# Optimization experiments

Measured on AMD Instinct MI355X. Metric: run time of the kernel, lower is better.

## Reference

```python
import jax, jax.numpy as jnp
import numpy as np

B, S, T = 64, 128, 64
HD, VS, VT = 1024, 32000, 32000


def setup_inputs() -> dict:
    key = jax.random.key(0)
    ks = jax.random.split(key, 20)
    p = lambda k, shape: (jax.random.normal(k, shape, jnp.float32) * 0.02)
    return {
        "src_nums": jax.random.randint(ks[0], (B, S), 0, VS, dtype=jnp.int32),
        "tgt_nums": jax.random.randint(ks[1], (B, T), 0, VT, dtype=jnp.int32),
        "src_emb": p(ks[2], (VS, HD)),
        "tgt_emb": p(ks[3], (VT, HD)),
        "enc_Wx1": p(ks[4], (HD, 4 * HD)),
        "enc_Wh1": p(ks[5], (HD, 4 * HD)),
        "enc_b1": jnp.zeros((4 * HD,), jnp.float32),
        "enc_Wx2": p(ks[6], (HD, 4 * HD)),
        "enc_Wh2": p(ks[7], (HD, 4 * HD)),
        "enc_b2": jnp.zeros((4 * HD,), jnp.float32),
        "dec_Wx": p(ks[8], (HD, 4 * HD)),
        "dec_Wh": p(ks[9], (HD, 4 * HD)),
        "dec_b": jnp.zeros((4 * HD,), jnp.float32),
        "dec_h0": p(ks[10], (1, HD)),
        "dec_m0": p(ks[11], (1, HD)),
        "Wt": p(ks[12], (2 * HD, HD)),
        "bt": jnp.zeros((HD,), jnp.float32),
        "Wo": p(ks[13], (HD, VT)),
        "bo": jnp.zeros((VT,), jnp.float32),
    }


def _lstm_cell(x, h, c, Wx, Wh, b):
    g = x @ Wx + h @ Wh + b            # [B, 4H], gate order i,f,g,o
    i, f, gg, o = jnp.split(g, 4, axis=-1)
    c = jax.nn.sigmoid(f) * c + jax.nn.sigmoid(i) * jnp.tanh(gg)
    h = jax.nn.sigmoid(o) * jnp.tanh(c)
    return h, c


def reference(src_nums, tgt_nums, src_emb, tgt_emb,
              enc_Wx1, enc_Wh1, enc_b1, enc_Wx2, enc_Wh2, enc_b2,
              dec_Wx, dec_Wh, dec_b, dec_h0, dec_m0, Wt, bt, Wo, bo):
    Bb, Ss = src_nums.shape
    Hd = src_emb.shape[1]
    # ---- Encoder: 2-layer LSTM over source ----
    embs = src_emb[src_nums]                       # [B,S,H]
    z0 = jnp.zeros((Bb, Hd), embs.dtype)

    def enc_step(carry, x):
        h1, c1, h2, c2 = carry
        h1, c1 = _lstm_cell(x, h1, c1, enc_Wx1, enc_Wh1, enc_b1)
        h2, c2 = _lstm_cell(h1, h2, c2, enc_Wx2, enc_Wh2, enc_b2)
        return (h1, c1, h2, c2), h2

    _, Hseq = jax.lax.scan(enc_step, (z0, z0, z0, z0), jnp.swapaxes(embs, 0, 1))
    Henc = jnp.swapaxes(Hseq, 0, 1)                # [B,S,H]
    mask = src_nums == 0                           # pad mask
    scale = 1.0 / jnp.sqrt(jnp.array(Hd, jnp.float32))

    # ---- Decoder: per-step attention + LSTMCell + tanh proj + log-softmax ----
    h = jnp.tile(dec_h0, (Bb, 1))
    m = jnp.tile(dec_m0, (Bb, 1))

    def dec_step(carry, tgt):
        h, m, loss = carry
        scores = jnp.einsum('bd,bsd->bs', h, Henc) * scale
        scores = jnp.where(mask, -jnp.inf, scores)
        a = jax.nn.softmax(scores, axis=-1)
        ctx = jnp.einsum('bs,bsd->bd', a, Henc)
        z = jnp.tanh(jnp.concatenate([ctx, h], axis=-1) @ Wt + bt)
        logp = jax.nn.log_softmax(z @ Wo + bo, axis=-1)    # [B,V]
        tok_lp = jnp.take_along_axis(logp, tgt[:, None], axis=-1)[:, 0]
        loss = loss - jnp.sum(jnp.where(tgt != 0, tok_lp, 0.0))
        x = tgt_emb[tgt]
        h, m = _lstm_cell(x, h, m, dec_Wx, dec_Wh, dec_b)
        return (h, m, loss), None

    (_, _, loss), _ = jax.lax.scan(
        dec_step, (h, m, jnp.float32(0.0)), jnp.swapaxes(tgt_nums, 0, 1))
    return loss
```

## Files before the change

kernel.cpp:

```cpp
#include <hip/hip_runtime.h>


#define Bv 64
#define Sv 128
#define Tv 64
#define Hv 1024
#define H4v 4096
#define Vv 32000
#define NBLK 256

using bf16x8 = __attribute__((ext_vector_type(8))) short;
using f32x4  = __attribute__((ext_vector_type(4))) float;

typedef __attribute__((address_space(1))) const void gvoid_t;
typedef __attribute__((address_space(3))) void lvoid_t;

__device__ __forceinline__ void gload16(const void* g, void* l) {
  __builtin_amdgcn_global_load_lds((gvoid_t*)g, (lvoid_t*)l, 16, 0, 0);
}

__device__ __forceinline__ float bf2f(unsigned short u) {
  unsigned int v = ((unsigned int)u) << 16;
  return __uint_as_float(v);
}
__device__ __forceinline__ unsigned short f2bf(float f) {
  unsigned int u = __float_as_uint(f);
  return (unsigned short)((u + 0x7FFFu + ((u >> 16) & 1u)) >> 16);
}
__device__ __forceinline__ float sigm(float x) { return 1.f / (1.f + __expf(-x)); }
__device__ __forceinline__ float tanh_f(float x) {
  float ax = fabsf(x);
  float e = __expf(-2.f * ax);
  float t = (1.f - e) / (1.f + e);
  return copysignf(t, x);
}

__device__ __forceinline__ int4 ldx4(const unsigned short* p) {
  int4 r;
  asm volatile("global_load_dwordx4 %0, %1, off" : "=v"(r) : "v"(p));
  return r;
}
__device__ __forceinline__ int2 ldx2(const unsigned short* p) {
  int2 r;
  asm volatile("global_load_dwordx2 %0, %1, off" : "=v"(r) : "v"(p));
  return r;
}
__device__ __forceinline__ void st_u16_wt(unsigned short* p, unsigned v) {
  asm volatile("global_store_short %0, %1, off sc0 sc1" :: "v"(p), "v"(v) : "memory");
}
__device__ __forceinline__ void vm_wait(int n) {
  if (n >= 12)     asm volatile("s_waitcnt vmcnt(12)" ::: "memory");
  else if (n >= 8) asm volatile("s_waitcnt vmcnt(8)" ::: "memory");
  else if (n >= 4) asm volatile("s_waitcnt vmcnt(4)" ::: "memory");
  else             asm volatile("s_waitcnt vmcnt(0)" ::: "memory");
}

__device__ __forceinline__ void wait_cnt(int* c, int target, int tid) {
  if (tid == 0) {
    int it = 0;
    while (__hip_atomic_load(c, __ATOMIC_RELAXED, __HIP_MEMORY_SCOPE_AGENT) < target) {
      __builtin_amdgcn_s_sleep(1);
      if (++it > (1 << 20)) break;
    }
  }
  __syncthreads();
}
__device__ __forceinline__ void post_cnt(int* c, int tid) {
  __syncthreads();
  if (tid == 0)
    __hip_atomic_fetch_add(c, 1, __ATOMIC_RELAXED, __HIP_MEMORY_SCOPE_AGENT);
}

__global__ __launch_bounds__(256) void transpose_bf16(const float* __restrict__ in,
                                                      unsigned short* __restrict__ out,
                                                      int R, int C, int ostride) {
  __shared__ float tile[32][33];
  int tx = threadIdx.x, ty = threadIdx.y;
  int c0 = blockIdx.x * 32, r0 = blockIdx.y * 32;
#pragma unroll
  for (int i = 0; i < 32; i += 8)
    tile[ty + i][tx] = in[(size_t)(r0 + ty + i) * C + c0 + tx];
  __syncthreads();
#pragma unroll
  for (int i = 0; i < 32; i += 8)
    out[(size_t)(c0 + ty + i) * ostride + r0 + tx] = f2bf(tile[tx][ty + i]);
}

__global__ __launch_bounds__(256) void gather_emb(const int* __restrict__ toks,
                                                  const float* __restrict__ emb,
                                                  unsigned short* __restrict__ dst) {
  int r = blockIdx.x, tid = threadIdx.x;
  int tok = toks[r];
  int j = tid * 4;
  float4 v = *(const float4*)&emb[(size_t)tok * Hv + j];
  ushort4 o;
  o.x = f2bf(v.x); o.y = f2bf(v.y); o.z = f2bf(v.z); o.w = f2bf(v.w);
  *(ushort4*)&dst[(size_t)r * Hv + j] = o;
}

__global__ __launch_bounds__(256) void init_k(unsigned short* __restrict__ zhx,
                                              unsigned short* __restrict__ hdx0,
                                              const float* __restrict__ h0,
                                              int* __restrict__ cnt) {
  int idx = blockIdx.x * 256 + threadIdx.x;
  int j = idx & (Hv - 1);
  int b = idx >> 10;
  zhx[idx] = 0;
  hdx0[(j >> 4) * 1024 + b * 16 + (j & 15)] = f2bf(h0[j]);
  if (idx < 6144) cnt[idx] = 0;
}

template <int EPI>
__global__ __launch_bounds__(256) void gemm128(const unsigned short* __restrict__ A,
                                               const unsigned short* __restrict__ Bt,
                                               const float* __restrict__ bias,
                                               unsigned short* __restrict__ Cbf,
                                               int M, int N, int K,
                                               float* __restrict__ partial,
                                               float* __restrict__ tlog,
                                               const int* __restrict__ tgt) {
  __shared__ unsigned short As[128 * 64];
  __shared__ unsigned short Bs[128 * 64];
  int tid = threadIdx.x, lane = tid & 63, w = tid >> 6;
  int wr = w >> 1, wc = w & 1;
  int m0 = blockIdx.y * 128, n0 = blockIdx.x * 128;
  f32x4 acc[4][4] = {};
  for (int k0 = 0; k0 < K; k0 += 64) {
    __syncthreads();
#pragma unroll
    for (int q = 0; q < 4; ++q) {
      int idx = q * 256 + tid;
      int row = idx >> 3, phys = idx & 7, lg = phys ^ (row & 7);
      gload16(A + (size_t)(m0 + row) * K + k0 + lg * 8, &As[idx * 8]);
    }
#pragma unroll
    for (int q = 0; q < 4; ++q) {
      int idx = q * 256 + tid;
      int row = idx >> 3, phys = idx & 7, lg = phys ^ (row & 7);
      gload16(Bt + (size_t)(n0 + row) * K + k0 + lg * 8, &Bs[idx * 8]);
    }
    __syncthreads();
#pragma unroll
    for (int kk = 0; kk < 64; kk += 32) {
      int lgb = (kk >> 3) + (lane >> 4);
      bf16x8 af[4], bfr[4];
#pragma unroll
      for (int m = 0; m < 4; ++m) {
        int row = wr * 64 + m * 16 + (lane & 15);
        af[m] = *(const bf16x8*)&As[(row * 8 + (lgb ^ (row & 7))) * 8];
      }
#pragma unroll
      for (int n = 0; n < 4; ++n) {
        int row = wc * 64 + n * 16 + (lane & 15);
        bfr[n] = *(const bf16x8*)&Bs[(row * 8 + (lgb ^ (row & 7))) * 8];
      }
#pragma unroll
      for (int m = 0; m < 4; ++m)
#pragma unroll
        for (int n = 0; n < 4; ++n)
          acc[m][n] = __builtin_amdgcn_mfma_f32_16x16x32_bf16(af[m], bfr[n], acc[m][n], 0, 0, 0);
    }
  }
  if (EPI == 2) {
#pragma unroll
    for (int m = 0; m < 4; ++m)
#pragma unroll
      for (int n = 0; n < 4; ++n) {
        int col = n0 + wc * 64 + n * 16 + (lane & 15);
        float bv = bias[col];
#pragma unroll
        for (int j = 0; j < 4; ++j) {
          int row = m0 + wr * 64 + m * 16 + (lane >> 4) * 4 + j;
          float v = acc[m][n][j] + bv;
          Cbf[(size_t)row * N + col] = f2bf(tanhf(v));
        }
      }
  } else if (EPI == 3) {
    int chunk = (n0 + wc * 64) >> 6;
#pragma unroll
    for (int m = 0; m < 4; ++m)
#pragma unroll
      for (int j = 0; j < 4; ++j) {
        int row = m0 + wr * 64 + m * 16 + (lane >> 4) * 4 + j;
        int tv = tgt[row];
        float se = 0.f;
#pragma unroll
        for (int n = 0; n < 4; ++n) {
          int col = n0 + wc * 64 + n * 16 + (lane & 15);
          float v = acc[m][n][j] + bias[col];
          se += __expf(v);
          if (col == tv) tlog[row] = v;
        }
        se += __shfl_xor(se, 1);
        se += __shfl_xor(se, 2);
        se += __shfl_xor(se, 4);
        se += __shfl_xor(se, 8);
        if ((lane & 15) == 0) partial[(size_t)chunk * M + row] = se;
      }
  } else {
    constexpr int TTc = (EPI == 4) ? 128 : 64;
#pragma unroll
    for (int m = 0; m < 4; ++m)
#pragma unroll
      for (int n = 0; n < 4; ++n) {
        int col = n0 + wc * 64 + n * 16 + (lane & 15);
        float bv = bias[col];
        int hcol = col & 1023, g = col >> 10;
#pragma unroll
        for (int j = 0; j < 4; ++j) {
          int row = m0 + wr * 64 + m * 16 + (lane >> 4) * 4 + j;
          int t = row % TTc, b = row / TTc;
          float v = acc[m][n][j] + bv;
          Cbf[((((size_t)t * 64 + (hcol >> 4)) * 64 + b) * 16 + (hcol & 15)) * 4 + g] = f2bf(v);
        }
      }
  }
}

template <int GRP>
__device__ __forceinline__ void run4(
    int gid, int tid, const unsigned short* __restrict__ Wg,
    const unsigned short* __restrict__ XPC, const float* __restrict__ eb2,
    const float* __restrict__ m0, const unsigned short* __restrict__ ZHX,
    unsigned short* __restrict__ H1X, unsigned short* __restrict__ H2X,
    unsigned short* __restrict__ HDX,
    int* __restrict__ C1, int* __restrict__ C2, int* __restrict__ CD,
    unsigned short* Wl, float* gl) {
  constexpr int COLS = (GRP == 1) ? 8 : 16;
  constexpr int KD   = (GRP == 1) ? 2048 : 1024;
  constexpr int NKS  = KD / 128;
  constexpr int NFR  = (GRP == 1) ? 2 : 4;
  constexpr int NT   = (GRP == 2) ? 63 : 128;
  constexpr int GPR  = KD / 8;
  constexpr int WROWS = 4 * COLS;
  const int lane = tid & 63, w = tid >> 6, l4 = lane >> 4, l15 = lane & 15;
  const int j0 = gid * COLS;

#pragma unroll
  for (int it = 0; it < (WROWS * GPR) / 256; ++it) {
    int L = it * 256 + tid;
    int row = L / GPR;
    int g = (L % GPR) ^ (row & 7);
    int gate = row / COLS, cl = row % COLS;
    gload16(Wg + (size_t)(gate * 1024 + j0 + cl) * KD + g * 8, Wl + (size_t)L * 8);
  }
  const int rr0 = (GRP == 1) ? (tid >> 3) : (tid >> 4);
  const int cc  = (GRP == 1) ? (tid & 7) : (tid & 15);
  const bool cellact = (GRP != 1) || (tid < 128);
  float cst[4];
#pragma unroll
  for (int c = 0; c < 4; ++c) cst[c] = (GRP == 2) ? m0[j0 + cc] : 0.f;
  float br_[4];
  if (GRP == 1) {
#pragma unroll
    for (int g = 0; g < 4; ++g) br_[g] = eb2[g * 1024 + j0 + cc];
  }
  const int kq16 = w * (KD / 32);

  asm volatile("s_waitcnt vmcnt(0)" ::: "memory");
  __syncthreads();

  for (int t = 0; t < NT; ++t) {
    if (GRP == 0) {
      if (t > 0) wait_cnt(C1 + (t - 1) * 16, 64, tid);
    } else if (GRP == 1) {
      wait_cnt(C1 + t * 16, 64, tid);
      if (t > 0) wait_cnt(C2 + (t - 1) * 16, 128, tid);
    } else {
      if (t > 0) wait_cnt(CD + t * 16, 64, tid);
    }
    const unsigned short* slab;
    int jb;
    if (GRP == 0) {
      slab = (t == 0) ? ZHX : H1X + (size_t)(t - 1) * 65536;
      jb = w * 256;
    } else if (GRP == 2) {
      slab = HDX + (size_t)t * 65536;
      jb = w * 256;
    } else {
      if (w < 2) { slab = H1X + (size_t)t * 65536; jb = w * 512; }
      else {
        slab = (t == 0) ? ZHX : H2X + (size_t)(t - 1) * 65536;
        jb = w * 512 - 1024;
      }
    }
    int2 xq[4];
    if (GRP != 1) {
      const unsigned short* xb = XPC + (((size_t)t * 64 + gid) * 64) * 64;
#pragma unroll
      for (int c = 0; c < 4; ++c)
        xq[c] = ldx2(xb + ((c * 16 + rr0) * 16 + cc) * 4);
    }
    const unsigned short* rp[4];
#pragma unroll
    for (int m = 0; m < 4; ++m)
      rp[m] = slab + (size_t)((jb >> 4) + (l4 >> 1)) * 1024 + (m * 16 + l15) * 16 + (l4 & 1) * 8;
    int4 afr[3][4];
#pragma unroll
    for (int pk = 0; pk < 3; ++pk)
#pragma unroll
      for (int m = 0; m < 4; ++m) afr[pk][m] = ldx4(rp[m] + pk * 2048);
    if (GRP != 1) vm_wait(12);
    bf16x8 wb[2][NFR];
#pragma unroll
    for (int n = 0; n < NFR; ++n) {
      int row = n * 16 + l15;
      wb[0][n] = *(const bf16x8*)&Wl[(size_t)row * KD + (size_t)((kq16 + l4) ^ (row & 7)) * 8];
    }
    f32x4 acc[4][NFR] = {};
#pragma unroll
    for (int ks = 0; ks < NKS; ++ks) {
      if (ks + 1 < NKS) {
#pragma unroll
        for (int n = 0; n < NFR; ++n) {
          int row = n * 16 + l15;
          wb[(ks + 1) & 1][n] = *(const bf16x8*)&Wl[(size_t)row * KD +
              (size_t)((kq16 + (ks + 1) * 4 + l4) ^ (row & 7)) * 8];
        }
      }
      int nrem = 4 * (NKS - 1 - ks);
      vm_wait(nrem > 8 ? 8 : nrem);
      __builtin_amdgcn_sched_barrier(0);
#pragma unroll
      for (int m = 0; m < 4; ++m)
#pragma unroll
        for (int n = 0; n < NFR; ++n)
          acc[m][n] = __builtin_amdgcn_mfma_f32_16x16x32_bf16(
              *(const bf16x8*)&afr[ks % 3][m], wb[ks & 1][n], acc[m][n], 0, 0, 0);
      if (ks + 3 < NKS) {
#pragma unroll
        for (int m = 0; m < 4; ++m) afr[ks % 3][m] = ldx4(rp[m] + (ks + 3) * 2048);
      }
    }
    unsigned short* outp;
    if (GRP == 0)      outp = H1X + (size_t)t * 65536 + gid * 1024;
    else if (GRP == 2) outp = HDX + (size_t)(t + 1) * 65536 + gid * 1024;
    else               outp = H2X + (size_t)t * 65536 + (size_t)(j0 >> 4) * 1024 + (j0 & 8);
#pragma unroll
    for (int c = 0; c < 4; ++c) {
#pragma unroll
      for (int n = 0; n < NFR; ++n)
#pragma unroll
        for (int j = 0; j < 4; ++j) {
          int ric = l4 * 4 + j;
          int col = n * 16 + l15;
          gl[(w * 16 + ric) * 64 + (col ^ ((ric * 4) & 63))] = acc[c][n][j];
        }
      __syncthreads();
      if (cellact) {
        float G[4];
#pragma unroll
        for (int g = 0; g < 4; ++g) {
          int sw = (g * COLS + cc) ^ ((rr0 * 4) & 63);
          G[g] = gl[(0 * 16 + rr0) * 64 + sw] + gl[(1 * 16 + rr0) * 64 + sw] +
                 gl[(2 * 16 + rr0) * 64 + sw] + gl[(3 * 16 + rr0) * 64 + sw];
        }
        float gi, gf, gg, go;
        if (GRP == 1) {
          gi = G[0] + br_[0]; gf = G[1] + br_[1]; gg = G[2] + br_[2]; go = G[3] + br_[3];
        } else {
          gi = G[0] + bf2f((unsigned short)(xq[c].x & 0xFFFF));
          gf = G[1] + bf2f((unsigned short)((unsigned)xq[c].x >> 16));
          gg = G[2] + bf2f((unsigned short)(xq[c].y & 0xFFFF));
          go = G[3] + bf2f((unsigned short)((unsigned)xq[c].y >> 16));
        }
        float cn = sigm(gf) * cst[c] + sigm(gi) * tanh_f(gg);
        float hn = sigm(go) * tanh_f(cn);
        cst[c] = cn;
        st_u16_wt(outp + (c * 16 + rr0) * 16 + cc, (unsigned)f2bf(hn));
      }
      __syncthreads();
    }
    asm volatile("s_waitcnt vmcnt(0)" ::: "memory");
    if (GRP == 0)      post_cnt(C1 + t * 16, tid);
    else if (GRP == 1) post_cnt(C2 + t * 16, tid);
    else               post_cnt(CD + (t + 1) * 16, tid);
  }
}

__global__ __launch_bounds__(256, 1) void chain_kernel(
    const unsigned short* __restrict__ W1T, const unsigned short* __restrict__ W2S,
    const unsigned short* __restrict__ WDT, const unsigned short* __restrict__ XPC1,
    const unsigned short* __restrict__ XPCD, const float* __restrict__ eb2,
    const float* __restrict__ m0, const unsigned short* __restrict__ ZHX,
    unsigned short* __restrict__ H1X, unsigned short* __restrict__ H2X,
    unsigned short* __restrict__ HDX, int* __restrict__ cnt) {
  __shared__ unsigned short Wl[65536];
  __shared__ float gl[4 * 16 * 64];
  int bid = blockIdx.x, tid = threadIdx.x;
  int* C1 = cnt;
  int* C2 = cnt + 160 * 16;
  int* CD = cnt + 320 * 16;
  if (bid < 64)
    run4<0>(bid, tid, W1T, XPC1, eb2, m0, ZHX, H1X, H2X, HDX, C1, C2, CD, Wl, gl);
  else if (bid < 192)
    run4<1>(bid - 64, tid, W2S, nullptr, eb2, m0, ZHX, H1X, H2X, HDX, C1, C2, CD, Wl, gl);
  else
    run4<2>(bid - 192, tid, WDT, XPCD, eb2, m0, ZHX, H1X, H2X, HDX, C1, C2, CD, Wl, gl);
}

__global__ __launch_bounds__(256) void reshape_h(const unsigned short* __restrict__ H2X,
                                                 const unsigned short* __restrict__ HDX,
                                                 unsigned short* __restrict__ HENC,
                                                 unsigned short* __restrict__ HDEC) {
  int row = blockIdx.x, tid = threadIdx.x;
  int g = tid >> 2, c = (tid & 3) * 4;
  if (row < Bv * Sv) {
    int b = row >> 7, s = row & 127;
    ushort4 v = *(const ushort4*)&H2X[(size_t)s * 65536 + g * 1024 + b * 16 + c];
    *(ushort4*)&HENC[(size_t)row * Hv + tid * 4] = v;
  } else {
    int r2 = row - Bv * Sv;
    int b = r2 >> 6, t = r2 & 63;
    ushort4 v = *(const ushort4*)&HDX[(size_t)t * 65536 + g * 1024 + b * 16 + c];
    *(ushort4*)&HDEC[(size_t)r2 * Hv + tid * 4] = v;
  }
}

__global__ __launch_bounds__(256) void attn_kernel(const unsigned short* __restrict__ Hdec,
                                                   const unsigned short* __restrict__ Henc,
                                                   const int* __restrict__ src_nums,
                                                   unsigned short* __restrict__ cat) {
  __shared__ float hd[Hv];
  __shared__ float sc[Sv];
  __shared__ float al[Sv];
  __shared__ float inv_s;
  int r = blockIdx.x;
  int b = r >> 6;
  int tid = threadIdx.x;
#pragma unroll
  for (int i = 0; i < 4; ++i) {
    int j = i * 256 + tid;
    hd[j] = bf2f(Hdec[(size_t)r * Hv + j]);
  }
  __syncthreads();
  int lane = tid & 63, w = tid >> 6;
  {
    int s = w * 32 + (lane >> 1);
    int half = lane & 1;
    const unsigned short* hrow = Henc + ((size_t)(b * Sv + s)) * Hv + half * 512;
    const float* hdp = hd + half * 512;
    float ps = 0.f;
#pragma unroll 8
    for (int j = 0; j < 512; j += 2) {
      unsigned int u = *(const unsigned int*)&hrow[j];
      ps += hdp[j] * bf2f((unsigned short)(u & 0xFFFFu));
      ps += hdp[j + 1] * bf2f((unsigned short)(u >> 16));
    }
    ps += __shfl_xor(ps, 1);
    if (half == 0) {
      float v = ps * 0.03125f;
      if (src_nums[b * Sv + s] == 0) v = -1e30f;
      sc[s] = v;
    }
  }
  __syncthreads();
  if (w == 0) {
    float v0 = sc[lane], v1 = sc[lane + 64];
    float mx = fmaxf(v0, v1);
#pragma unroll
    for (int o = 1; o < 64; o <<= 1) mx = fmaxf(mx, __shfl_xor(mx, o));
    float e0 = __expf(v0 - mx), e1 = __expf(v1 - mx);
    al[lane] = e0;
    al[lane + 64] = e1;
    float ss = e0 + e1;
#pragma unroll
    for (int o = 1; o < 64; o <<= 1) ss += __shfl_xor(ss, o);
    if (lane == 0) inv_s = 1.f / ss;
  }
  __syncthreads();
  float inv = inv_s;
  int j0 = tid * 4;
  float a0 = 0, a1 = 0, a2 = 0, a3 = 0;
  for (int s2 = 0; s2 < Sv; ++s2) {
    float a = al[s2];
    const unsigned short* hr = Henc + ((size_t)(b * Sv + s2)) * Hv + j0;
    ushort4 u = *(const ushort4*)hr;
    a0 += a * bf2f(u.x);
    a1 += a * bf2f(u.y);
    a2 += a * bf2f(u.z);
    a3 += a * bf2f(u.w);
  }
  ushort4 o4;
  o4.x = f2bf(a0 * inv); o4.y = f2bf(a1 * inv); o4.z = f2bf(a2 * inv); o4.w = f2bf(a3 * inv);
  *(ushort4*)&cat[(size_t)r * 2048 + j0] = o4;
  ushort4 h4;
  h4.x = f2bf(hd[j0]); h4.y = f2bf(hd[j0 + 1]); h4.z = f2bf(hd[j0 + 2]); h4.w = f2bf(hd[j0 + 3]);
  *(ushort4*)&cat[(size_t)r * 2048 + 1024 + j0] = h4;
}

__global__ __launch_bounds__(256) void loss_row(const float* __restrict__ partial,
                                                const float* __restrict__ tlog,
                                                const int* __restrict__ tgt,
                                                float* __restrict__ rowloss) {
  int r = blockIdx.x * 256 + threadIdx.x;
  float ssum = 0.f;
  for (int c = 0; c < Vv / 64; ++c) ssum += partial[(size_t)c * (Bv * Tv) + r];
  float l = logf(ssum) - tlog[r];
  rowloss[r] = (tgt[r] != 0) ? l : 0.f;
}

__global__ __launch_bounds__(256) void loss_final(const float* __restrict__ rowloss,
                                                  float* __restrict__ out) {
  __shared__ float red[256];
  int tid = threadIdx.x;
  float s = 0.f;
  for (int i = tid; i < Bv * Tv; i += 256) s += rowloss[i];
  red[tid] = s;
  __syncthreads();
  for (int o = 128; o > 0; o >>= 1) {
    if (tid < o) red[tid] += red[tid + o];
    __syncthreads();
  }
  if (tid == 0) out[0] = red[0];
}

extern "C" void kernel_launch(void* const* d_in, const int* in_sizes, int n_in,
                              void* d_out, int out_size, void* d_ws, size_t ws_size,
                              hipStream_t stream) {
  (void)in_sizes; (void)n_in; (void)out_size; (void)ws_size;
  const int* src_nums = (const int*)d_in[0];
  const int* tgt_nums = (const int*)d_in[1];
  const float* src_emb = (const float*)d_in[2];
  const float* tgt_emb = (const float*)d_in[3];
  const float* eWx1 = (const float*)d_in[4];
  const float* eWh1 = (const float*)d_in[5];
  const float* eb1  = (const float*)d_in[6];
  const float* eWx2 = (const float*)d_in[7];
  const float* eWh2 = (const float*)d_in[8];
  const float* eb2  = (const float*)d_in[9];
  const float* dWx  = (const float*)d_in[10];
  const float* dWh  = (const float*)d_in[11];
  const float* db   = (const float*)d_in[12];
  const float* h0   = (const float*)d_in[13];
  const float* m0   = (const float*)d_in[14];
  const float* Wt   = (const float*)d_in[15];
  const float* bt   = (const float*)d_in[16];
  const float* Wo   = (const float*)d_in[17];
  const float* bo   = (const float*)d_in[18];

  char* base = (char*)d_ws;
  size_t off = 0;
  auto alloc = [&](size_t bytes) -> void* {
    void* r = base + off;
    off += (bytes + 255) & ~(size_t)255;
    return r;
  };
  unsigned short* WX1T = (unsigned short*)alloc((size_t)H4v * Hv * 2);
  unsigned short* W1T  = (unsigned short*)alloc((size_t)H4v * Hv * 2);
  unsigned short* W2S  = (unsigned short*)alloc((size_t)H4v * 2048 * 2);
  unsigned short* DWXT = (unsigned short*)alloc((size_t)H4v * Hv * 2);
  unsigned short* WDT  = (unsigned short*)alloc((size_t)H4v * Hv * 2);
  unsigned short* WTT  = (unsigned short*)alloc((size_t)Hv * 2048 * 2);
  unsigned short* WOT  = (unsigned short*)alloc((size_t)Vv * Hv * 2);
  unsigned short* SEMB = (unsigned short*)alloc((size_t)Bv * Sv * Hv * 2);
  unsigned short* TEMB = (unsigned short*)alloc((size_t)Bv * Tv * Hv * 2);
  unsigned short* XPC1 = (unsigned short*)alloc((size_t)Bv * Sv * H4v * 2);
  unsigned short* XPCD = (unsigned short*)alloc((size_t)Bv * Tv * H4v * 2);
  unsigned short* HENC = (unsigned short*)alloc((size_t)Bv * Sv * Hv * 2);
  unsigned short* HDEC = (unsigned short*)alloc((size_t)Bv * Tv * Hv * 2);
  unsigned short* H1X  = (unsigned short*)alloc((size_t)Sv * Bv * Hv * 2);
  unsigned short* H2X  = (unsigned short*)alloc((size_t)Sv * Bv * Hv * 2);
  unsigned short* HDX  = (unsigned short*)alloc((size_t)Tv * Bv * Hv * 2);
  unsigned short* ZHX  = (unsigned short*)alloc((size_t)Bv * Hv * 2);
  unsigned short* CAT  = (unsigned short*)alloc((size_t)Bv * Tv * 2048 * 2);
  unsigned short* ZBUF = (unsigned short*)alloc((size_t)Bv * Tv * Hv * 2);
  float* PART  = (float*)alloc((size_t)(Vv / 64) * (Bv * Tv) * 4);
  float* TLOG  = (float*)alloc((size_t)(Bv * Tv) * 4);
  float* RLOSS = (float*)alloc((size_t)(Bv * Tv) * 4);
  int* CNT     = (int*)alloc(6144 * 4);

  dim3 tb(32, 8);
  transpose_bf16<<<dim3(H4v / 32, Hv / 32), tb, 0, stream>>>(eWx1, WX1T, Hv, H4v, Hv);
  transpose_bf16<<<dim3(H4v / 32, Hv / 32), tb, 0, stream>>>(eWh1, W1T, Hv, H4v, Hv);
  transpose_bf16<<<dim3(H4v / 32, Hv / 32), tb, 0, stream>>>(eWx2, W2S, Hv, H4v, 2048);
  transpose_bf16<<<dim3(H4v / 32, Hv / 32), tb, 0, stream>>>(eWh2, W2S + 1024, Hv, H4v, 2048);
  transpose_bf16<<<dim3(H4v / 32, Hv / 32), tb, 0, stream>>>(dWx, DWXT, Hv, H4v, Hv);
  transpose_bf16<<<dim3(H4v / 32, Hv / 32), tb, 0, stream>>>(dWh, WDT, Hv, H4v, Hv);
  transpose_bf16<<<dim3(Hv / 32, 2048 / 32), tb, 0, stream>>>(Wt, WTT, 2048, Hv, 2048);
  transpose_bf16<<<dim3(Vv / 32, Hv / 32), tb, 0, stream>>>(Wo, WOT, Hv, Vv, Hv);

  init_k<<<256, 256, 0, stream>>>(ZHX, HDX, h0, CNT);
  gather_emb<<<Bv * Sv, 256, 0, stream>>>(src_nums, src_emb, SEMB);
  gather_emb<<<Bv * Tv, 256, 0, stream>>>(tgt_nums, tgt_emb, TEMB);

  gemm128<4><<<dim3(H4v / 128, (Bv * Sv) / 128), 256, 0, stream>>>(
      SEMB, WX1T, eb1, XPC1, Bv * Sv, H4v, Hv, nullptr, nullptr, nullptr);
  gemm128<5><<<dim3(H4v / 128, (Bv * Tv) / 128), 256, 0, stream>>>(
      TEMB, DWXT, db, XPCD, Bv * Tv, H4v, Hv, nullptr, nullptr, nullptr);

  chain_kernel<<<NBLK, 256, 0, stream>>>(W1T, W2S, WDT, XPC1, XPCD, eb2, m0, ZHX, H1X, H2X,
                                         HDX, CNT);

  reshape_h<<<Bv * Sv + Bv * Tv, 256, 0, stream>>>(H2X, HDX, HENC, HDEC);

  attn_kernel<<<Bv * Tv, 256, 0, stream>>>(HDEC, HENC, src_nums, CAT);
  gemm128<2><<<dim3(Hv / 128, (Bv * Tv) / 128), 256, 0, stream>>>(
      CAT, WTT, bt, ZBUF, Bv * Tv, Hv, 2048, nullptr, nullptr, nullptr);
  gemm128<3><<<dim3(Vv / 128, (Bv * Tv) / 128), 256, 0, stream>>>(
      ZBUF, WOT, bo, nullptr, Bv * Tv, Vv, Hv, PART, TLOG, tgt_nums);
  loss_row<<<(Bv * Tv) / 256, 256, 0, stream>>>(PART, TLOG, tgt_nums, RLOSS);
  loss_final<<<1, 256, 0, stream>>>(RLOSS, (float*)d_out);
}
```

Baseline: 1.828 ms.

## Split encoder layer 2 into separate input and recurrent groups with per-block flags

The persistent chain kernel's layer-2 encoder work is split into two 64-block groups. One computes the recurrent h2@Wh2 partial gates into an fp32 buffer, and the other adds the h1@Wx2 product, bias and that partial, then applies the cell. This shortens the per-step K dimension from 2048 to 1024 for both groups, so their work can overlap. Cross-block synchronisation moves from shared atomic counters with sleep to per-producer flags, which 64 lanes poll with a wave-wide all-check. The cost is extra global traffic for the partial gates, more flag memory, and a tighter spin loop with a smaller timeout.

Result: slower. 2.361 ms (+29.1%).

```diff
diff --git a/kernel.cpp b/kernel.cpp
--- a/kernel.cpp
+++ b/kernel.cpp
@@ -45,30 +45,46 @@
   asm volatile("global_load_dwordx2 %0, %1, off" : "=v"(r) : "v"(p));
   return r;
 }
+__device__ __forceinline__ int4 ldx4_cv(const void* p) {
+  int4 r;
+  asm volatile("global_load_dwordx4 %0, %1, off sc0 sc1" : "=v"(r) : "v"(p));
+  return r;
+}
 __device__ __forceinline__ void st_u16_wt(unsigned short* p, unsigned v) {
   asm volatile("global_store_short %0, %1, off sc0 sc1" :: "v"(p), "v"(v) : "memory");
 }
+__device__ __forceinline__ void stx2_wt(float* p, int2 v) {
+  asm volatile("global_store_dwordx2 %0, %1, off sc0 sc1" :: "v"(p), "v"(v) : "memory");
+}
 __device__ __forceinline__ void vm_wait(int n) {
-  if (n >= 12)     asm volatile("s_waitcnt vmcnt(12)" ::: "memory");
-  else if (n >= 8) asm volatile("s_waitcnt vmcnt(8)" ::: "memory");
+  if (n >= 8)      asm volatile("s_waitcnt vmcnt(8)" ::: "memory");
   else if (n >= 4) asm volatile("s_waitcnt vmcnt(4)" ::: "memory");
   else             asm volatile("s_waitcnt vmcnt(0)" ::: "memory");
 }
 
-__device__ __forceinline__ void wait_cnt(int* c, int target, int tid) {
+__device__ __forceinline__ void wait_all64(int* f, int tid) {
+  if (tid < 64) {
+    int it = 0;
+    while (true) {
+      int v = __hip_atomic_load(f + tid, __ATOMIC_RELAXED, __HIP_MEMORY_SCOPE_AGENT);
+      if (__all(v != 0)) break;
+      if (++it > (1 << 17)) break;
+    }
+  }
+  __syncthreads();
+}
+__device__ __forceinline__ void wait_one(int* f, int tid) {
   if (tid == 0) {
     int it = 0;
-    while (__hip_atomic_load(c, __ATOMIC_RELAXED, __HIP_MEMORY_SCOPE_AGENT) < target) {
-      __builtin_amdgcn_s_sleep(1);
-      if (++it > (1 << 20)) break;
-    }
-  }
-  __syncthreads();
-}
-__device__ __forceinline__ void post_cnt(int* c, int tid) {
-  __syncthreads();
-  if (tid == 0)
-    __hip_atomic_fetch_add(c, 1, __ATOMIC_RELAXED, __HIP_MEMORY_SCOPE_AGENT);
+    while (__hip_atomic_load(f, __ATOMIC_RELAXED, __HIP_MEMORY_SCOPE_AGENT) == 0) {
+      if (++it > (1 << 17)) break;
+    }
+  }
+  __syncthreads();
+}
+__device__ __forceinline__ void post_flag(int* f, int tid) {
+  __syncthreads();
+  if (tid == 0) __hip_atomic_store(f, 1, __ATOMIC_RELAXED, __HIP_MEMORY_SCOPE_AGENT);
 }
 
 __global__ __launch_bounds__(256) void transpose_bf16(const float* __restrict__ in,
@@ -101,13 +117,13 @@
 __global__ __launch_bounds__(256) void init_k(unsigned short* __restrict__ zhx,
                                               unsigned short* __restrict__ hdx0,
                                               const float* __restrict__ h0,
-                                              int* __restrict__ cnt) {
+                                              int* __restrict__ flg) {
   int idx = blockIdx.x * 256 + threadIdx.x;
   int j = idx & (Hv - 1);
   int b = idx >> 10;
   zhx[idx] = 0;
   hdx0[(j >> 4) * 1024 + b * 16 + (j & 15)] = f2bf(h0[j]);
-  if (idx < 6144) cnt[idx] = 0;
+  if (idx < 28672) flg[idx] = 0;
 }
 
 template <int EPI>
@@ -218,103 +234,86 @@
 }
 
 template <int GRP>
-__device__ __forceinline__ void run4(
-    int gid, int tid, const unsigned short* __restrict__ Wg,
+__device__ __forceinline__ void run5(
+    int gid, int tid, const unsigned short* __restrict__ Wg, int wstride, int koff,
     const unsigned short* __restrict__ XPC, const float* __restrict__ eb2,
     const float* __restrict__ m0, const unsigned short* __restrict__ ZHX,
     unsigned short* __restrict__ H1X, unsigned short* __restrict__ H2X,
-    unsigned short* __restrict__ HDX,
-    int* __restrict__ C1, int* __restrict__ C2, int* __restrict__ CD,
-    unsigned short* Wl, float* gl) {
-  constexpr int COLS = (GRP == 1) ? 8 : 16;
-  constexpr int KD   = (GRP == 1) ? 2048 : 1024;
-  constexpr int NKS  = KD / 128;
-  constexpr int NFR  = (GRP == 1) ? 2 : 4;
-  constexpr int NT   = (GRP == 2) ? 63 : 128;
-  constexpr int GPR  = KD / 8;
-  constexpr int WROWS = 4 * COLS;
+    unsigned short* __restrict__ HDX, float* __restrict__ PG,
+    int* __restrict__ C1, int* __restrict__ C2A, int* __restrict__ C2B,
+    int* __restrict__ CD, unsigned short* Wl, float* gl) {
+  constexpr int NT = (GRP == 3) ? 63 : 128;
+  constexpr int NKS = 8;
   const int lane = tid & 63, w = tid >> 6, l4 = lane >> 4, l15 = lane & 15;
-  const int j0 = gid * COLS;
-
-#pragma unroll
-  for (int it = 0; it < (WROWS * GPR) / 256; ++it) {
+  const int j0 = gid * 16;
+
+#pragma unroll
+  for (int it = 0; it < 32; ++it) {
     int L = it * 256 + tid;
-    int row = L / GPR;
-    int g = (L % GPR) ^ (row & 7);
-    int gate = row / COLS, cl = row % COLS;
-    gload16(Wg + (size_t)(gate * 1024 + j0 + cl) * KD + g * 8, Wl + (size_t)L * 8);
-  }
-  const int rr0 = (GRP == 1) ? (tid >> 3) : (tid >> 4);
-  const int cc  = (GRP == 1) ? (tid & 7) : (tid & 15);
-  const bool cellact = (GRP != 1) || (tid < 128);
+    int row = L >> 7;
+    int g = (L & 127) ^ (row & 7);
+    int gate = row >> 4, cl = row & 15;
+    gload16(Wg + (size_t)(gate * 1024 + j0 + cl) * wstride + koff + g * 8, Wl + (size_t)L * 8);
+  }
+  const int rr0 = tid >> 4, cc = tid & 15;
   float cst[4];
 #pragma unroll
-  for (int c = 0; c < 4; ++c) cst[c] = (GRP == 2) ? m0[j0 + cc] : 0.f;
+  for (int c = 0; c < 4; ++c) cst[c] = (GRP == 3) ? m0[j0 + cc] : 0.f;
   float br_[4];
   if (GRP == 1) {
 #pragma unroll
     for (int g = 0; g < 4; ++g) br_[g] = eb2[g * 1024 + j0 + cc];
   }
-  const int kq16 = w * (KD / 32);
-
+  const int kq16 = w * 32;
   asm volatile("s_waitcnt vmcnt(0)" ::: "memory");
   __syncthreads();
 
   for (int t = 0; t < NT; ++t) {
-    if (GRP == 0) {
-      if (t > 0) wait_cnt(C1 + (t - 1) * 16, 64, tid);
+    if (GRP == 0)      { if (t > 0) wait_all64(C1 + (t - 1) * 64, tid); }
+    else if (GRP == 1) { wait_all64(C1 + t * 64, tid); wait_one(C2B + t * 64 + gid, tid); }
+    else if (GRP == 2) { if (t > 0) wait_all64(C2A + (t - 1) * 64, tid); }
+    else               { if (t > 0) wait_all64(CD + t * 64, tid); }
+
+    const unsigned short* slab;
+    if (GRP == 0)      slab = (t == 0) ? ZHX : H1X + (size_t)(t - 1) * 65536;
+    else if (GRP == 1) slab = H1X + (size_t)t * 65536;
+    else if (GRP == 2) slab = (t == 0) ? ZHX : H2X + (size_t)(t - 1) * 65536;
+    else               slab = HDX + (size_t)t * 65536;
+
+    int2 xq[4];
+    int4 pgi[4];
+    if (GRP == 0 || GRP == 3) {
+      const unsigned short* xb = XPC + ((size_t)t * 64 + gid) * 4096;
+#pragma unroll
+      for (int c = 0; c < 4; ++c) xq[c] = ldx2(xb + ((c * 16 + rr0) * 16 + cc) * 4);
     } else if (GRP == 1) {
-      wait_cnt(C1 + t * 16, 64, tid);
-      if (t > 0) wait_cnt(C2 + (t - 1) * 16, 128, tid);
-    } else {
-      if (t > 0) wait_cnt(CD + t * 16, 64, tid);
-    }
-    const unsigned short* slab;
-    int jb;
-    if (GRP == 0) {
-      slab = (t == 0) ? ZHX : H1X + (size_t)(t - 1) * 65536;
-      jb = w * 256;
-    } else if (GRP == 2) {
-      slab = HDX + (size_t)t * 65536;
-      jb = w * 256;
-    } else {
-      if (w < 2) { slab = H1X + (size_t)t * 65536; jb = w * 512; }
-      else {
-        slab = (t == 0) ? ZHX : H2X + (size_t)(t - 1) * 65536;
-        jb = w * 512 - 1024;
-      }
-    }
-    int2 xq[4];
-    if (GRP != 1) {
-      const unsigned short* xb = XPC + (((size_t)t * 64 + gid) * 64) * 64;
-#pragma unroll
-      for (int c = 0; c < 4; ++c)
-        xq[c] = ldx2(xb + ((c * 16 + rr0) * 16 + cc) * 4);
+      const float* pb = PG + (size_t)gid * 4096;
+#pragma unroll
+      for (int c = 0; c < 4; ++c) pgi[c] = ldx4_cv(pb + ((c * 16 + rr0) * 16 + cc) * 4);
     }
     const unsigned short* rp[4];
 #pragma unroll
     for (int m = 0; m < 4; ++m)
-      rp[m] = slab + (size_t)((jb >> 4) + (l4 >> 1)) * 1024 + (m * 16 + l15) * 16 + (l4 & 1) * 8;
+      rp[m] = slab + (size_t)(w * 16 + (l4 >> 1)) * 1024 + (m * 16 + l15) * 16 + (l4 & 1) * 8;
     int4 afr[3][4];
 #pragma unroll
     for (int pk = 0; pk < 3; ++pk)
 #pragma unroll
       for (int m = 0; m < 4; ++m) afr[pk][m] = ldx4(rp[m] + pk * 2048);
-    if (GRP != 1) vm_wait(12);
-    bf16x8 wb[2][NFR];
-#pragma unroll
-    for (int n = 0; n < NFR; ++n) {
+    bf16x8 wb[2][4];
+#pragma unroll
+    for (int n = 0; n < 4; ++n) {
       int row = n * 16 + l15;
-      wb[0][n] = *(const bf16x8*)&Wl[(size_t)row * KD + (size_t)((kq16 + l4) ^ (row & 7)) * 8];
-    }
-    f32x4 acc[4][NFR] = {};
+      wb[0][n] = *(const bf16x8*)&Wl[(size_t)row * 1024 + (size_t)((kq16 + l4) ^ (row & 7)) * 8];
+    }
+    f32x4 acc[4][4] = {};
 #pragma unroll
     for (int ks = 0; ks < NKS; ++ks) {
       if (ks + 1 < NKS) {
 #pragma unroll
-        for (int n = 0; n < NFR; ++n) {
+        for (int n = 0; n < 4; ++n) {
           int row = n * 16 + l15;
-          wb[(ks + 1) & 1][n] = *(const bf16x8*)&Wl[(size_t)row * KD +
+          wb[(ks + 1) & 1][n] = *(const bf16x8*)&Wl[(size_t)row * 1024 +
               (size_t)((kq16 + (ks + 1) * 4 + l4) ^ (row & 7)) * 8];
         }
       }
@@ -324,7 +323,7 @@
 #pragma unroll
       for (int m = 0; m < 4; ++m)
 #pragma unroll
-        for (int n = 0; n < NFR; ++n)
+        for (int n = 0; n < 4; ++n)
           acc[m][n] = __builtin_amdgcn_mfma_f32_16x16x32_bf16(
               *(const bf16x8*)&afr[ks % 3][m], wb[ks & 1][n], acc[m][n], 0, 0, 0);
       if (ks + 3 < NKS) {
@@ -332,14 +331,16 @@
         for (int m = 0; m < 4; ++m) afr[ks % 3][m] = ldx4(rp[m] + (ks + 3) * 2048);
       }
     }
-    unsigned short* outp;
+    unsigned short* outp = nullptr;
+    float* outpf = nullptr;
     if (GRP == 0)      outp = H1X + (size_t)t * 65536 + gid * 1024;
-    else if (GRP == 2) outp = HDX + (size_t)(t + 1) * 65536 + gid * 1024;
-    else               outp = H2X + (size_t)t * 65536 + (size_t)(j0 >> 4) * 1024 + (j0 & 8);
+    else if (GRP == 1) outp = H2X + (size_t)t * 65536 + gid * 1024;
+    else if (GRP == 3) outp = HDX + (size_t)(t + 1) * 65536 + gid * 1024;
+    else               outpf = PG + (size_t)gid * 4096;
 #pragma unroll
     for (int c = 0; c < 4; ++c) {
 #pragma unroll
-      for (int n = 0; n < NFR; ++n)
+      for (int n = 0; n < 4; ++n)
 #pragma unroll
         for (int j = 0; j < 4; ++j) {
           int ric = l4 * 4 + j;
@@ -347,34 +348,47 @@
           gl[(w * 16 + ric) * 64 + (col ^ ((ric * 4) & 63))] = acc[c][n][j];
         }
       __syncthreads();
-      if (cellact) {
+      {
         float G[4];
 #pragma unroll
         for (int g = 0; g < 4; ++g) {
-          int sw = (g * COLS + cc) ^ ((rr0 * 4) & 63);
+          int sw = (g * 16 + cc) ^ ((rr0 * 4) & 63);
           G[g] = gl[(0 * 16 + rr0) * 64 + sw] + gl[(1 * 16 + rr0) * 64 + sw] +
                  gl[(2 * 16 + rr0) * 64 + sw] + gl[(3 * 16 + rr0) * 64 + sw];
         }
-        float gi, gf, gg, go;
-        if (GRP == 1) {
-          gi = G[0] + br_[0]; gf = G[1] + br_[1]; gg = G[2] + br_[2]; go = G[3] + br_[3];
+        if (GRP == 2) {
+          int2 pv0, pv1;
+          pv0.x = __float_as_int(G[0]); pv0.y = __float_as_int(G[1]);
+          pv1.x = __float_as_int(G[2]); pv1.y = __float_as_int(G[3]);
+          float* pp = outpf + ((c * 16 + rr0) * 16 + cc) * 4;
+          stx2_wt(pp, pv0);
+          stx2_wt(pp + 2, pv1);
         } else {
-          gi = G[0] + bf2f((unsigned short)(xq[c].x & 0xFFFF));
-          gf = G[1] + bf2f((unsigned short)((unsigned)xq[c].x >> 16));
-          gg = G[2] + bf2f((unsigned short)(xq[c].y & 0xFFFF));
-          go = G[3] + bf2f((unsigned short)((unsigned)xq[c].y >> 16));
+          float gi, gf, gg, go;
+          if (GRP == 1) {
+            gi = G[0] + __int_as_float(pgi[c].x) + br_[0];
+            gf = G[1] + __int_as_float(pgi[c].y) + br_[1];
+            gg = G[2] + __int_as_float(pgi[c].z) + br_[2];
+            go = G[3] + __int_as_float(pgi[c].w) + br_[3];
+          } else {
+            gi = G[0] + bf2f((unsigned short)(xq[c].x & 0xFFFF));
+            gf = G[1] + bf2f((unsigned short)((unsigned)xq[c].x >> 16));
+            gg = G[2] + bf2f((unsigned short)(xq[c].y & 0xFFFF));
+            go = G[3] + bf2f((unsigned short)((unsigned)xq[c].y >> 16));
+          }
+          float cn = sigm(gf) * cst[c] + sigm(gi) * tanh_f(gg);
+          float hn = sigm(go) * tanh_f(cn);
+          cst[c] = cn;
+          st_u16_wt(outp + (c * 16 + rr0) * 16 + cc, (unsigned)f2bf(hn));
         }
-        float cn = sigm(gf) * cst[c] + sigm(gi) * tanh_f(gg);
-        float hn = sigm(go) * tanh_f(cn);
-        cst[c] = cn;
-        st_u16_wt(outp + (c * 16 + rr0) * 16 + cc, (unsigned)f2bf(hn));
       }
       __syncthreads();
     }
     asm volatile("s_waitcnt vmcnt(0)" ::: "memory");
-    if (GRP == 0)      post_cnt(C1 + t * 16, tid);
-    else if (GRP == 1) post_cnt(C2 + t * 16, tid);
-    else               post_cnt(CD + (t + 1) * 16, tid);
+    if (GRP == 0)      post_flag(C1 + t * 64 + gid, tid);
+    else if (GRP == 1) post_flag(C2A + t * 64 + gid, tid);
+    else if (GRP == 2) post_flag(C2B + t * 64 + gid, tid);
+    else               post_flag(CD + (t + 1) * 64 + gid, tid);
   }
 }
 
@@ -384,19 +398,26 @@
     const unsigned short* __restrict__ XPCD, const float* __restrict__ eb2,
     const float* __restrict__ m0, const unsigned short* __restrict__ ZHX,
     unsigned short* __restrict__ H1X, unsigned short* __restrict__ H2X,
-    unsigned short* __restrict__ HDX, int* __restrict__ cnt) {
+    unsigned short* __restrict__ HDX, float* __restrict__ PG, int* __restrict__ flg) {
   __shared__ unsigned short Wl[65536];
   __shared__ float gl[4 * 16 * 64];
   int bid = blockIdx.x, tid = threadIdx.x;
-  int* C1 = cnt;
-  int* C2 = cnt + 160 * 16;
-  int* CD = cnt + 320 * 16;
+  int* C1  = flg;
+  int* C2A = flg + 8192;
+  int* C2B = flg + 16384;
+  int* CD  = flg + 24576;
   if (bid < 64)
-    run4<0>(bid, tid, W1T, XPC1, eb2, m0, ZHX, H1X, H2X, HDX, C1, C2, CD, Wl, gl);
+    run5<0>(bid, tid, W1T, 1024, 0, XPC1, nullptr, nullptr, ZHX, H1X, H2X, HDX, PG,
+            C1, C2A, C2B, CD, Wl, gl);
+  else if (bid < 128)
+    run5<1>(bid - 64, tid, W2S, 2048, 0, nullptr, eb2, nullptr, ZHX, H1X, H2X, HDX, PG,
+            C1, C2A, C2B, CD, Wl, gl);
   else if (bid < 192)
-    run4<1>(bid - 64, tid, W2S, nullptr, eb2, m0, ZHX, H1X, H2X, HDX, C1, C2, CD, Wl, gl);
+    run5<2>(bid - 128, tid, W2S, 2048, 1024, nullptr, nullptr, nullptr, ZHX, H1X, H2X, HDX, PG,
+            C1, C2A, C2B, CD, Wl, gl);
   else
-    run4<2>(bid - 192, tid, WDT, XPCD, eb2, m0, ZHX, H1X, H2X, HDX, C1, C2, CD, Wl, gl);
+    run5<3>(bid - 192, tid, WDT, 1024, 0, XPCD, nullptr, m0, ZHX, H1X, H2X, HDX, PG,
+            C1, C2A, C2B, CD, Wl, gl);
 }
 
 __global__ __launch_bounds__(256) void reshape_h(const unsigned short* __restrict__ H2X,
@@ -568,7 +589,8 @@
   float* PART  = (float*)alloc((size_t)(Vv / 64) * (Bv * Tv) * 4);
   float* TLOG  = (float*)alloc((size_t)(Bv * Tv) * 4);
   float* RLOSS = (float*)alloc((size_t)(Bv * Tv) * 4);
-  int* CNT     = (int*)alloc(6144 * 4);
+  float* PG    = (float*)alloc((size_t)64 * 4096 * 4);
+  int* FLG     = (int*)alloc(28672 * 4);
 
   dim3 tb(32, 8);
   transpose_bf16<<<dim3(H4v / 32, Hv / 32), tb, 0, stream>>>(eWx1, WX1T, Hv, H4v, Hv);
@@ -580,7 +602,7 @@
   transpose_bf16<<<dim3(Hv / 32, 2048 / 32), tb, 0, stream>>>(Wt, WTT, 2048, Hv, 2048);
   transpose_bf16<<<dim3(Vv / 32, Hv / 32), tb, 0, stream>>>(Wo, WOT, Hv, Vv, Hv);
 
-  init_k<<<256, 256, 0, stream>>>(ZHX, HDX, h0, CNT);
+  init_k<<<256, 256, 0, stream>>>(ZHX, HDX, h0, FLG);
   gather_emb<<<Bv * Sv, 256, 0, stream>>>(src_nums, src_emb, SEMB);
   gather_emb<<<Bv * Tv, 256, 0, stream>>>(tgt_nums, tgt_emb, TEMB);
 
@@ -590,7 +612,7 @@
       TEMB, DWXT, db, XPCD, Bv * Tv, H4v, Hv, nullptr, nullptr, nullptr);
 
   chain_kernel<<<NBLK, 256, 0, stream>>>(W1T, W2S, WDT, XPC1, XPCD, eb2, m0, ZHX, H1X, H2X,
-                                         HDX, CNT);
+                                         HDX, PG, FLG);
 
   reshape_h<<<Bv * Sv + Bv * Tv, 256, 0, stream>>>(H2X, HDX, HENC, HDEC);
 
```
